# Performance work log

Hardware: AMD Instinct MI355X
Metric: run time of the kernel (lower is better)

## Reference

```python
import jax, jax.numpy as jnp
import numpy as np

NEG = -9999.0      # chart init / clip floor (np.clip a_min=-9999.0)
THRESH = -9000.0   # 'pseudo_score > -9000' acceptance gate
ARC_BONUS = 5.0    # '+ 5' added to every arc candidate


def _fill_chart(vinfo):
    """Eisner DP chart fill, faithful to the sequential numpy triple loop.
    vinfo: [N, N] arc scores. Returns (score_chart [N,N,2,2], backtrace [N,N,2,2]).
    Chart axes: [i, j, direction, completeness] as in the torch source.
    Parallelized over span start i and split q; sequential over width k via scan.
    Sequential-update subtleties of the original q-loop are reproduced exactly:
      * complete (0,1) at q=i reads the (0,0) cell as it stands after only the
        q=i incomplete update ('part00');
      * complete (1,1) at q=j reads the fully updated (1,0) cell ('new10');
      * complete (0,1) at q=j and (1,1) at q=i are strict-improvement no-ops;
      * ties keep the earliest q (jnp.argmax returns first occurrence).
    """
    N = vinfo.shape[0]
    idx = jnp.arange(N)
    ii = idx[:, None]   # span start i
    mm = idx[None, :]   # split offset m; q = i + m
    S = jnp.full((N, N, 2, 2), NEG, dtype=vinfo.dtype).at[idx, idx].set(0.0)
    BT = jnp.zeros((N, N, 2, 2), dtype=jnp.int32)

    def step(carry, k):
        S, BT = carry
        j = idx + k
        row_ok = j < N
        okb = row_ok[:, None]
        jc = jnp.minimum(j, N - 1)
        jb = jc[:, None]
        q = ii + mm
        qc = jnp.minimum(q, N - 1)
        q1c = jnp.minimum(q + 1, N - 1)

        # ---- incomplete spans (0,0) and (1,0): q in [i, j-1]  <=>  m in [0, k-1]
        base = jnp.where((mm < k) & okb,
                         S[:, :, 1, 1][ii, qc] + S[:, :, 0, 1][q1c, jb],
                         -jnp.inf)                      # [N (i), N (m)]
        vL = vinfo[jc, idx][:, None]   # vinfo[j, i] -> arc j<-...: head j
        vR = vinfo[idx, jc][:, None]   # vinfo[i, j]
        p00 = jnp.maximum(base + vL + ARC_BONUS, NEG)
        p10 = jnp.maximum(base + vR + ARC_BONUS, NEG)
        m00 = jnp.max(p00, axis=1); q00 = idx + jnp.argmax(p00, axis=1)
        m10 = jnp.max(p10, axis=1); q10 = idx + jnp.argmax(p10, axis=1)
        ok00 = row_ok & (m00 > THRESH)
        ok10 = row_ok & (m10 > THRESH)
        # chart[i,j,0,0] as it stands right after the q=i iteration
        part00 = jnp.where(row_ok & (p00[:, 0] > THRESH), p00[:, 0], NEG)
        new10 = jnp.where(ok10, m10, NEG)

        m_mid = (mm >= 1) & (mm < k) & okb
        # ---- complete (0,1): q=i uses partially built (0,0); q=j is a no-op
        c01 = jnp.where(m_mid, S[:, :, 0, 1][ii, qc] + S[:, :, 0, 0][qc, jb], -jnp.inf)
        c01 = c01.at[:, 0].set(jnp.where(row_ok, part00, -jnp.inf))
        p01 = jnp.maximum(c01, NEG)
        m01 = jnp.max(p01, axis=1); q01 = idx + jnp.argmax(p01, axis=1)
        ok01 = row_ok & (m01 > THRESH)

        # ---- complete (1,1): q=i is a no-op; q=j uses freshly updated (1,0)
        c11 = jnp.where(m_mid, S[:, :, 1, 0][ii, qc] + S[:, :, 1, 1][qc, jb], -jnp.inf)
        c11 = jnp.where((mm == k) & okb, new10[:, None], c11)
        p11 = jnp.maximum(c11, NEG)
        m11 = jnp.max(p11, axis=1); q11 = idx + jnp.argmax(p11, axis=1)
        ok11 = row_ok & (m11 > THRESH)

        def upd(S, BT, a, b, ok, val, qarg):
            S = S.at[idx, jc, a, b].set(jnp.where(ok, val, S[idx, jc, a, b]))
            BT = BT.at[idx, jc, a, b].set(
                jnp.where(ok, qarg, BT[idx, jc, a, b]).astype(jnp.int32))
            return S, BT

        S, BT = upd(S, BT, 0, 0, ok00, m00, q00)
        S, BT = upd(S, BT, 1, 0, ok10, m10, q10)
        S, BT = upd(S, BT, 0, 1, ok01, m01, q01)
        S, BT = upd(S, BT, 1, 1, ok11, m11, q11)
        return (S, BT), None

    (S, BT), _ = jax.lax.scan(step, (S, BT), jnp.arange(1, N))
    return S, BT


def setup_inputs() -> dict:
    key = jax.random.key(0)
    B, N = 64, 128
    b_vinfo_mtx = jax.random.normal(key, (B, N, N), dtype=jnp.float32)
    b_buffer_size = jnp.full((B,), N, dtype=jnp.int32)
    return {"b_vinfo_mtx": b_vinfo_mtx, "b_buffer_size": b_buffer_size}


def reference(b_vinfo_mtx, b_buffer_size):
    # All sentences use the full buffer (b_buffer_size == N), so the batch is
    # processed as one vmapped chart fill.
    scores, backtrace = jax.vmap(_fill_chart)(b_vinfo_mtx)
    return scores, backtrace
```

## Files before the change

kernel.cpp:

```cpp
#include <hip/hip_runtime.h>
#include <stdint.h>

static constexpr int kN = 128;
static constexpr int kTri = (kN * (kN - 1)) / 2;
static constexpr int kTriD = (kN * (kN + 1)) / 2;
static constexpr int kThreads = 1024;
static constexpr float kNeg = -9999.0f;
static constexpr float kThresh = -9000.0f;
static constexpr float kArcBonus = 5.0f;
static constexpr int kDynLds = kTriD * 16;
static constexpr int kCMax = 9;
static constexpr int kSer = 28;
static constexpr int kStride = 64 - kSer;

__device__ __forceinline__ int rowBase(int i) { return (i * (2 * kN - 1 - i)) / 2; }
__device__ __forceinline__ int colBaseD(int c) { return (c * (c + 1)) / 2; }

__device__ __forceinline__ void ldsBarrier() {
    asm volatile("s_waitcnt lgkmcnt(0)\n\ts_barrier" ::: "memory");
}

template <int CTRL>
__device__ __forceinline__ float dppMax(float x) {
    const int y = __builtin_amdgcn_update_dpp(__float_as_int(x), __float_as_int(x),
                                              CTRL, 0xF, 0xF, true);
    return fmaxf(x, __int_as_float(y));
}
template <int CTRL>
__device__ __forceinline__ int dppMinI(int x) {
    const int y = __builtin_amdgcn_update_dpp(x, x, CTRL, 0xF, 0xF, true);
    return (y < x) ? y : x;
}
template <int P>
__device__ __forceinline__ float grpMax(float x) {
    float r = dppMax<0xB1>(x);
    if constexpr (P >= 4) r = dppMax<0x4E>(r);
    if constexpr (P >= 8) r = dppMax<0x141>(r);
    if constexpr (P >= 16) r = dppMax<0x140>(r);
    return r;
}
template <int P>
__device__ __forceinline__ int grpMinI(int x) {
    int r = dppMinI<0xB1>(x);
    if constexpr (P >= 4) r = dppMinI<0x4E>(r);
    if constexpr (P >= 8) r = dppMinI<0x141>(r);
    if constexpr (P >= 16) r = dppMinI<0x140>(r);
    return r;
}

__device__ __forceinline__ float4 writeCell(float4* __restrict__ Q4,
                                            uint32_t* __restrict__ wsBT,
                                            int qjb, int i, int wsIdx, int k,
                                            float gb, int ib, float vLc, float vRc,
                                            float v01, int i01, float v11, int i11) {
    const float v00 = (gb + vLc) + kArcBonus;
    const float v10 = (gb + vRc) + kArcBonus;
    const float new10 = (v10 > kThresh) ? v10 : kNeg;
    if (new10 > v11) { v11 = new10; i11 = k; }
    float4 w = make_float4(kNeg, kNeg, kNeg, kNeg);
    uint32_t p = 0;
    if (v00 > kThresh) { w.x = v00; p |= (uint32_t)(i + ib); }
    if (v01 > kThresh) { w.z = v01; p |= (uint32_t)(i + i01) << 8; }
    if (v10 > kThresh) { w.w = v10; p |= (uint32_t)(i + ib) << 16; }
    if (v11 > kThresh) { w.y = v11; p |= (uint32_t)(i + i11) << 24; }
    Q4[qjb + i] = w;
    wsBT[wsIdx] = p;
    return w;
}

__device__ __forceinline__ void doStepSerialNB(int k, int lam, int i,
                                               float4* __restrict__ Q4,
                                               uint32_t* __restrict__ wsBT,
                                               int& j, int& qjb, int rbi,
                                               const float*& pL, const float*& pR,
                                               float& vL, float& vR,
                                               float (&sr11)[kSer + 1], float (&sr01)[kSer + 1],
                                               float (&sr10)[kSer + 1]) {
    const bool act = (lam + k <= 63) && (i < kN - k);
    const float vLc = vL, vRc = vR;
    const int qjbc = qjb;
    float bmax = -3.0e38f, v01 = -3.0e38f, v11 = -3.0e38f;
    int ib = 0, i01 = 0, i11 = 0x7FFFFFFF;
    if (act) {
        float4 cur = Q4[qjbc + i + 1];
        bmax = cur.z; ib = 0;
        const float p00 = (cur.z + vLc) + kArcBonus;
        v01 = (p00 > kThresh) ? p00 : kNeg; i01 = 0;
#pragma unroll
        for (int m = 1; m < kSer; ++m) {
            if (m < k) {
                const float4 nxt = Q4[qjbc + i + m + 1];
                const float base = sr11[m] + nxt.z;
                const float p01v = sr01[m] + cur.x;
                const float p11v = sr10[m] + cur.y;
                if (base > bmax) { bmax = base; ib = m; }
                if (p01v > v01) { v01 = p01v; i01 = m; }
                if (p11v > v11) { v11 = p11v; i11 = m; }
                cur = nxt;
            }
        }
    }
    if (k < kSer) {
        const bool nact = (lam + k + 1 <= 63) && (i < kN - (k + 1));
        qjb += j + 1; ++j; pL += kN; ++pR;
        vL = nact ? *pL : 0.f;
        vR = nact ? *pR : 0.f;
    }
    if (act) {
        const float4 w = writeCell(Q4, wsBT, qjbc, i, rbi + k - 1, k,
                                   bmax, ib, vLc, vRc, v01, i01, v11, i11);
        sr11[k] = w.y; sr01[k] = w.z; sr10[k] = w.w;
    }
}

template <int LP, int C>
__device__ __forceinline__ void preloadRow(int k0, int tid,
                                           const float4* __restrict__ Q4,
                                           float (&r11)[kCMax], float (&r01)[kCMax],
                                           float (&r10)[kCMax]) {
    const int i = tid >> LP;
    const int l = tid & ((1 << LP) - 1);
    const int mlo = l * C;
    const int mstart = mlo ? mlo : 1;
    const bool act = i < (kN - k0);
#pragma unroll
    for (int c = 0; c < C; ++c) {
        const int m = mstart + c;
        if (act && (m < mlo + C) && (m <= k0 - 1)) {
            const float4 d = Q4[colBaseD(i + m) + i];
            r11[c] = d.y; r01[c] = d.z; r10[c] = d.w;
        }
    }
}

template <int LP, int C>
__device__ __forceinline__ void fwInit(int k0, int tid,
                                       const float (&r11)[kCMax], const float (&r01)[kCMax],
                                       const float (&r10)[kCMax],
                                       float& fw11, float& fw01, float& fw10) {
    const int l = tid & ((1 << LP) - 1);
    const int mlo = l * C;
    const int mstart = mlo ? mlo : 1;
#pragma unroll
    for (int c = 0; c < C; ++c) {
        if (mstart + c == k0 - 1) { fw11 = r11[c]; fw01 = r01[c]; fw10 = r10[c]; }
    }
}

template <int LP, int C>
__device__ __forceinline__ void doStepC(int k, int i, int l,
                                        float4* __restrict__ Q4,
                                        uint32_t* __restrict__ wsBT,
                                        int& j, int& qjb, int rbi,
                                        const float*& pL, const float*& pR,
                                        float& vL, float& vR,
                                        float (&r11)[kCMax], float (&r01)[kCMax],
                                        float (&r10)[kCMax],
                                        float& fw11, float& fw01, float& fw10) {
    constexpr int P = 1 << LP;
    static_assert(P <= 16, "reductions must stay pure-DPP");
    const bool act = i < kN - k;
    const float vLc = vL, vRc = vR;
    const int mlo = l * C;
    const int mstart = mlo ? mlo : 1;
    const int mhi = (mlo + C < k) ? (mlo + C) : k;
    const int qjbc = qjb;

    float bmax = -3.0e38f, v01 = -3.0e38f, v11 = -3.0e38f;
    int ib = 0x7FFFFFFF, i01 = 0x7FFFFFFF, i11 = 0x7FFFFFFF;

    const int mf = k - 1;
    const bool lact = act && (mstart < mhi);
    float4 cur = make_float4(0.f, 0.f, 0.f, 0.f);
    if (lact) cur = Q4[qjbc + i + mstart];
    if (act && mlo == 0) {
        bmax = cur.z; ib = 0;
        const float p00 = (cur.z + vLc) + kArcBonus;
        v01 = (p00 > kThresh) ? p00 : kNeg; i01 = 0;
    }
#pragma unroll
    for (int c = 0; c < C; ++c) {
        const int m = mstart + c;
        const bool isF = (m == mf);
        const float a11 = isF ? fw11 : r11[c];
        const float a01 = isF ? fw01 : r01[c];
        const float a10 = isF ? fw10 : r10[c];
        r11[c] = a11; r01[c] = a01; r10[c] = a10;
        const bool on = lact && (m < mhi);
        if (on) {
            const float4 nxt = Q4[qjbc + i + m + 1];
            const float base = a11 + nxt.z;
            const float p01v = a01 + cur.x;
            const float p11v = a10 + cur.y;
            if (base > bmax) { bmax = base; ib = m; }
            if (p01v > v01) { v01 = p01v; i01 = m; }
            if (p11v > v11) { v11 = p11v; i11 = m; }
            cur = nxt;
        }
    }

    {
        const bool nact = i < kN - (k + 1);
        qjb += j + 1; ++j; pL += kN; ++pR;
        vL = nact ? *pL : 0.f;
        vR = nact ? *pR : 0.f;
    }

    const float gB = grpMax<P>(bmax);
    const float g01 = grpMax<P>(v01);
    const float g11 = grpMax<P>(v11);
    int cB = (bmax == gB) ? ib : 0x7FFFFFFF;
    int c01 = (v01 == g01) ? i01 : 0x7FFFFFFF;
    int c11 = (v11 == g11) ? i11 : 0x7FFFFFFF;
    cB = grpMinI<P>(cB);
    c01 = grpMinI<P>(c01);
    c11 = grpMinI<P>(c11);

    const float v10f = (gB + vRc) + kArcBonus;
    const float new10 = (v10f > kThresh) ? v10f : kNeg;
    float v11m = g11;
    if (new10 > v11m) v11m = new10;
    fw11 = (v11m > kThresh) ? v11m : kNeg;
    fw01 = (g01 > kThresh) ? g01 : kNeg;
    fw10 = (v10f > kThresh) ? v10f : kNeg;

    if (act && l == 0) {
        writeCell(Q4, wsBT, qjbc, i, rbi + k - 1, k,
                  gB, cB, vLc, vRc, g01, c01, g11, c11);
    }
}

template <int LP, int C>
__device__ __forceinline__ void runPhaseC(int k0, int k1, int tid,
        float4* __restrict__ Q4, uint32_t* __restrict__ wsBT,
        const float* __restrict__ v,
        float (&r11)[kCMax], float (&r01)[kCMax], float (&r10)[kCMax]) {
    const int i = tid >> LP;
    const int l = tid & ((1 << LP) - 1);
    int j = i + k0;
    int qjb = colBaseD(j);
    const int rbi = rowBase(i & (kN - 1));
    const float* pL = v + (size_t)j * kN + i;
    const float* pR = v + (size_t)i * kN + j;
    const bool a0 = i < kN - k0;
    float vL = a0 ? *pL : 0.f;
    float vR = a0 ? *pR : 0.f;
    preloadRow<LP, C>(k0, tid, Q4, r11, r01, r10);
    float fw11 = kNeg, fw01 = kNeg, fw10 = kNeg;
    fwInit<LP, C>(k0, tid, r11, r01, r10, fw11, fw01, fw10);
    for (int k = k0; k < k1; ++k) {
        doStepC<LP, C>(k, i, l, Q4, wsBT, j, qjb, rbi, pL, pR, vL, vR,
                       r11, r01, r10, fw11, fw01, fw10);
        ldsBarrier();
    }
}

__global__ __launch_bounds__(kThreads) void eisner_dp(
    const float* __restrict__ vinfo,
    float* __restrict__ outS,
    float* __restrict__ outBT,
    uint32_t* __restrict__ btPacked)
{
    extern __shared__ float4 Q4[];

    const int tid = threadIdx.x;
    const int b = blockIdx.x;
    const float* v = vinfo + (size_t)b * kN * kN;
    uint32_t* wsBT = btPacked + (size_t)b * kTri;

    const float4 zeroq = make_float4(0.f, 0.f, 0.f, 0.f);
    if (tid < kN) Q4[colBaseD(tid) + tid] = zeroq;
    __syncthreads();

    if (tid < 4 * 64) {
        const int w = tid >> 6;
        const int lam = tid & 63;
        const int i = kStride * w + lam;
        const int ic = (i < kN) ? i : (kN - 1);
        float sr11[kSer + 1], sr01[kSer + 1], sr10[kSer + 1];
        int j = i + 1;
        int qjb = colBaseD((i + 1 < kN) ? i + 1 : kN - 1);
        const int rbi = rowBase(ic);
        const float* pL = v + (size_t)((i + 1 < kN) ? i + 1 : 0) * kN + ic;
        const float* pR = v + (size_t)ic * kN + ((i + 1 < kN) ? i + 1 : 0);
        const bool a0 = (lam + 1 <= 63) && (i < kN - 1);
        float vL = a0 ? *pL : 0.f;
        float vR = a0 ? *pR : 0.f;
#pragma unroll
        for (int k = 1; k <= kSer; ++k) {
            doStepSerialNB(k, lam, i, Q4, wsBT, j, qjb, rbi, pL, pR, vL, vR,
                           sr11, sr01, sr10);
            asm volatile("" ::: "memory");
        }
    }
    ldsBarrier();

    float r11[kCMax], r01[kCMax], r10[kCMax];
#pragma unroll
    for (int c = 0; c < kCMax; ++c) { r11[c] = kNeg; r01[c] = kNeg; r10[c] = kNeg; }

    runPhaseC<3, 5>(29, 40, tid, Q4, wsBT, v, r11, r01, r10);
    runPhaseC<3, 7>(40, 56, tid, Q4, wsBT, v, r11, r01, r10);
    runPhaseC<3, 9>(56, 64, tid, Q4, wsBT, v, r11, r01, r10);
    runPhaseC<4, 5>(64, 80, tid, Q4, wsBT, v, r11, r01, r10);
    runPhaseC<4, 7>(80, 112, tid, Q4, wsBT, v, r11, r01, r10);
    runPhaseC<4, 9>(112, 128, tid, Q4, wsBT, v, r11, r01, r10);

    __syncthreads();

    float4* gS4 = (float4*)(outS + (size_t)b * kN * kN * 4);
    float4* gB4 = (float4*)(outBT + (size_t)b * kN * kN * 4);
    const float4 negq = make_float4(kNeg, kNeg, kNeg, kNeg);
    for (int c = tid; c < kN * kN; c += kThreads) {
        const int i = c >> 7, j = c & (kN - 1);
        if (i < j) {
            const float4 q = Q4[colBaseD(j) + i];
            gS4[c] = make_float4(q.x, q.z, q.w, q.y);
            const uint32_t p = wsBT[rowBase(i) + (j - i - 1)];
            gB4[c] = make_float4((float)(p & 255u), (float)((p >> 8) & 255u),
                                 (float)((p >> 16) & 255u), (float)(p >> 24));
        } else if (i == j) {
            gS4[c] = zeroq;
            gB4[c] = zeroq;
        } else {
            gS4[c] = negq;
            gB4[c] = zeroq;
        }
    }
}

extern "C" void kernel_launch(void* const* d_in, const int* in_sizes, int n_in,
                              void* d_out, int out_size, void* d_ws, size_t ws_size,
                              hipStream_t stream) {
    (void)n_in; (void)out_size; (void)ws_size;
    const float* vinfo = (const float*)d_in[0];
    const int B = in_sizes[1];
    float* outS = (float*)d_out;
    float* outBT = outS + (size_t)B * kN * kN * 4;
    uint32_t* btPacked = (uint32_t*)d_ws;

    hipFuncSetAttribute(reinterpret_cast<const void*>(eisner_dp),
                        hipFuncAttributeMaxDynamicSharedMemorySize, kDynLds);

    eisner_dp<<<dim3(B), dim3(kThreads), kDynLds, stream>>>(vinfo, outS, outBT, btPacked);
}
```

Before: 247.3 us.

## Run final widths in a single wavefront and skip idle waves in phase C

Widths 112-127 now run in a new tail routine on a single 64-thread wavefront, 4 lanes per span start, with no block-wide barriers between steps. Phase C waves whose span rows are all finished skip the step work and only take part in the remaining barriers. The serial prologue is cut from 28 to 24 widths, so phase C starts at width 25. The aim is to remove barrier and idle-wave cost where few cells remain. In exchange each tail lane scans up to 32 splits in sequence.

```diff
diff --git a/kernel.cpp b/kernel.cpp
--- a/kernel.cpp
+++ b/kernel.cpp
@@ -10,8 +10,9 @@
 static constexpr float kArcBonus = 5.0f;
 static constexpr int kDynLds = kTriD * 16;
 static constexpr int kCMax = 9;
-static constexpr int kSer = 28;
-static constexpr int kStride = 64 - kSer;
+static constexpr int kSer = 24;
+static constexpr int kStride = 40;
+static constexpr int kTail = 112;
 
 __device__ __forceinline__ int rowBase(int i) { return (i * (2 * kN - 1 - i)) / 2; }
 __device__ __forceinline__ int colBaseD(int c) { return (c * (c + 1)) / 2; }
@@ -237,22 +238,102 @@
         float (&r11)[kCMax], float (&r01)[kCMax], float (&r10)[kCMax]) {
     const int i = tid >> LP;
     const int l = tid & ((1 << LP) - 1);
-    int j = i + k0;
-    int qjb = colBaseD(j);
-    const int rbi = rowBase(i & (kN - 1));
-    const float* pL = v + (size_t)j * kN + i;
-    const float* pR = v + (size_t)i * kN + j;
-    const bool a0 = i < kN - k0;
-    float vL = a0 ? *pL : 0.f;
-    float vR = a0 ? *pR : 0.f;
-    preloadRow<LP, C>(k0, tid, Q4, r11, r01, r10);
-    float fw11 = kNeg, fw01 = kNeg, fw10 = kNeg;
-    fwInit<LP, C>(k0, tid, r11, r01, r10, fw11, fw01, fw10);
-    for (int k = k0; k < k1; ++k) {
-        doStepC<LP, C>(k, i, l, Q4, wsBT, j, qjb, rbi, pL, pR, vL, vR,
-                       r11, r01, r10, fw11, fw01, fw10);
-        ldsBarrier();
-    }
+    const int firstGroup = (tid & ~63) >> LP;
+    int kEnd = kN - firstGroup;
+    if (kEnd > k1) kEnd = k1;
+    if (kEnd > k0) {
+        int j = i + k0;
+        int qjb = colBaseD(j);
+        const int rbi = rowBase(i & (kN - 1));
+        const float* pL = v + (size_t)j * kN + i;
+        const float* pR = v + (size_t)i * kN + j;
+        const bool a0 = i < kN - k0;
+        float vL = a0 ? *pL : 0.f;
+        float vR = a0 ? *pR : 0.f;
+        preloadRow<LP, C>(k0, tid, Q4, r11, r01, r10);
+        float fw11 = kNeg, fw01 = kNeg, fw10 = kNeg;
+        fwInit<LP, C>(k0, tid, r11, r01, r10, fw11, fw01, fw10);
+        for (int k = k0; k < kEnd; ++k) {
+            doStepC<LP, C>(k, i, l, Q4, wsBT, j, qjb, rbi, pL, pR, vL, vR,
+                           r11, r01, r10, fw11, fw01, fw10);
+            ldsBarrier();
+        }
+        for (int k = kEnd; k < k1; ++k) ldsBarrier();
+    } else {
+        for (int k = k0; k < k1; ++k) ldsBarrier();
+    }
+}
+
+__device__ __forceinline__ void runTail(int tid,
+        float4* __restrict__ Q4, uint32_t* __restrict__ wsBT,
+        const float* __restrict__ v) {
+    if (tid < 64) {
+        const int i = tid >> 2;
+        const int l = tid & 3;
+        const int rbi = rowBase(i);
+        int j = i + kTail;
+        int qjb = colBaseD(j);
+        const float* pL = v + (size_t)j * kN + i;
+        const float* pR = v + (size_t)i * kN + j;
+        float vL = *pL;
+        float vR = *pR;
+        for (int k = kTail; k < kN; ++k) {
+            const bool act = i < kN - k;
+            const float vLc = vL, vRc = vR;
+            const int qjbc = qjb;
+            const int mlo = l * 32;
+            const int mstart = mlo ? mlo : 1;
+            const int mhi = (mlo + 32 < k) ? (mlo + 32) : k;
+            float bmax = -3.0e38f, v01 = -3.0e38f, v11 = -3.0e38f;
+            int ib = 0x7FFFFFFF, i01 = 0x7FFFFFFF, i11 = 0x7FFFFFFF;
+            const bool lact = act && (mstart < mhi);
+            if (lact) {
+                int q = i + mstart;
+                float4 cur = Q4[qjbc + q];
+                if (mlo == 0) {
+                    bmax = cur.z; ib = 0;
+                    const float p00 = (cur.z + vLc) + kArcBonus;
+                    v01 = (p00 > kThresh) ? p00 : kNeg; i01 = 0;
+                }
+                int dA = colBaseD(q) + i;
+                int dInc = q + 1;
+#pragma unroll 8
+                for (int m = mstart; m < mhi; ++m) {
+                    const float4 nxt = Q4[qjbc + q + 1];
+                    const float4 diq = Q4[dA];
+                    const float base = diq.y + nxt.z;
+                    const float p01v = diq.z + cur.x;
+                    const float p11v = diq.w + cur.y;
+                    if (base > bmax) { bmax = base; ib = m; }
+                    if (p01v > v01) { v01 = p01v; i01 = m; }
+                    if (p11v > v11) { v11 = p11v; i11 = m; }
+                    cur = nxt;
+                    dA += dInc; ++dInc; ++q;
+                }
+            }
+            {
+                const bool nact = i < kN - (k + 1);
+                qjb += j + 1; ++j; pL += kN; ++pR;
+                vL = nact ? *pL : 0.f;
+                vR = nact ? *pR : 0.f;
+            }
+            const float gB = grpMax<4>(bmax);
+            const float g01 = grpMax<4>(v01);
+            const float g11 = grpMax<4>(v11);
+            int cB = (bmax == gB) ? ib : 0x7FFFFFFF;
+            int c01 = (v01 == g01) ? i01 : 0x7FFFFFFF;
+            int c11 = (v11 == g11) ? i11 : 0x7FFFFFFF;
+            cB = grpMinI<4>(cB);
+            c01 = grpMinI<4>(c01);
+            c11 = grpMinI<4>(c11);
+            if (act && l == 0) {
+                writeCell(Q4, wsBT, qjbc, i, rbi + k - 1, k,
+                          gB, cB, vLc, vRc, g01, c01, g11, c11);
+            }
+            asm volatile("" ::: "memory");
+        }
+    }
+    ldsBarrier();
 }
 
 __global__ __launch_bounds__(kThreads) void eisner_dp(
@@ -299,12 +380,13 @@
 #pragma unroll
     for (int c = 0; c < kCMax; ++c) { r11[c] = kNeg; r01[c] = kNeg; r10[c] = kNeg; }
 
-    runPhaseC<3, 5>(29, 40, tid, Q4, wsBT, v, r11, r01, r10);
+    runPhaseC<3, 5>(25, 40, tid, Q4, wsBT, v, r11, r01, r10);
     runPhaseC<3, 7>(40, 56, tid, Q4, wsBT, v, r11, r01, r10);
     runPhaseC<3, 9>(56, 64, tid, Q4, wsBT, v, r11, r01, r10);
     runPhaseC<4, 5>(64, 80, tid, Q4, wsBT, v, r11, r01, r10);
     runPhaseC<4, 7>(80, 112, tid, Q4, wsBT, v, r11, r01, r10);
-    runPhaseC<4, 9>(112, 128, tid, Q4, wsBT, v, r11, r01, r10);
+
+    runTail(tid, Q4, wsBT, v);
 
     __syncthreads();
 
```

New measurement: 248.9 us. About the same (+0.6%).
